# Kernel optimization log

Hardware: AMD Instinct MI355X
Metric: run time of the kernel (lower is better)

The kernel has to match this reference:

```python
import jax, jax.numpy as jnp
import numpy as np

N_NEURONS = 1024
TABLE_SIZE = 65536  # array_size (2048 quotients) * 2**remainder_size (32)
BATCH = 8192


def setup_inputs() -> dict:
    key = jax.random.key(0)
    k1, k2 = jax.random.split(key)
    # Input tuples: one fingerprint per neuron per sample, value = (quotient << rs) | remainder
    data = jax.random.randint(k1, (BATCH, N_NEURONS), 0, TABLE_SIZE, dtype=jnp.int32)
    # Dense membership/counter table equivalent to the fitted quotient filter state
    # (quotient filter with full remainders stored is an exact fingerprint set).
    table = jax.random.uniform(k2, (N_NEURONS, TABLE_SIZE), dtype=jnp.float32)
    return {"data": data, "table": table}


def reference(data, table):
    # check_member(neuron=j, quotient=data[i,j]>>rs, remainder=data[i,j]&mask)
    # == table[j, data[i,j]]; multi_rank sums memberships over neurons.
    neuron_idx = jnp.arange(table.shape[0])[None, :]          # [1, N]
    gathered = table[neuron_idx, data]                        # [B, N] gather
    response = jnp.sum(gathered, axis=1)                      # [B]
    return response
```

## Files before the change

kernel.cpp:

```cpp
#include <hip/hip_runtime.h>

#define N_NEURONS 1024
#define TABLE_SIZE 65536
#define BATCH 8192
#define NGROUPS 8
#define NPG 128
#define SPB 128
#define NCHUNK 8

__global__ __launch_bounds__(256) void qw_partial_kernel(
    const int* __restrict__ data,
    const float* __restrict__ table,
    float* __restrict__ part)
{
    const int b      = blockIdx.x;
    const int g      = b & (NGROUPS - 1);
    const int sub    = b >> 3;
    const int t      = threadIdx.x;
    const int h      = t & 1;
    const int sid    = t >> 1;
    const int sample = sub * SPB + sid;

    const int* __restrict__ dptr =
        data + (size_t)sample * N_NEURONS + g * NPG + h * 8;

    const float* __restrict__ tb =
        table + (size_t)(g * NPG + h * 8) * TABLE_SIZE;

    int4 i0 = *reinterpret_cast<const int4*>(dptr);
    int4 i1 = *reinterpret_cast<const int4*>(dptr + 4);

    float acc = 0.0f;
#pragma unroll
    for (int c = 0; c < NCHUNK; ++c) {
        const int4 c0 = i0;
        const int4 c1 = i1;
        if (c + 1 < NCHUNK) {
            const int* __restrict__ p = dptr + (c + 1) * 16;
            i0 = *reinterpret_cast<const int4*>(p);
            i1 = *reinterpret_cast<const int4*>(p + 4);
        }
        const float* __restrict__ tc = tb + (size_t)(c * 16) * TABLE_SIZE;
        const float v0 = tc[(size_t)0 * TABLE_SIZE + (size_t)c0.x];
        const float v1 = tc[(size_t)1 * TABLE_SIZE + (size_t)c0.y];
        const float v2 = tc[(size_t)2 * TABLE_SIZE + (size_t)c0.z];
        const float v3 = tc[(size_t)3 * TABLE_SIZE + (size_t)c0.w];
        const float v4 = tc[(size_t)4 * TABLE_SIZE + (size_t)c1.x];
        const float v5 = tc[(size_t)5 * TABLE_SIZE + (size_t)c1.y];
        const float v6 = tc[(size_t)6 * TABLE_SIZE + (size_t)c1.z];
        const float v7 = tc[(size_t)7 * TABLE_SIZE + (size_t)c1.w];
        acc += ((v0 + v1) + (v2 + v3)) + ((v4 + v5) + (v6 + v7));
        __syncthreads();
    }

    acc += __shfl_xor(acc, 1, 64);
    if (h == 0) {
        part[(size_t)g * BATCH + sample] = acc;
    }
}

__global__ __launch_bounds__(256) void qw_reduce_kernel(
    const float* __restrict__ part,
    float* __restrict__ out)
{
    const int i = blockIdx.x * 256 + threadIdx.x;
    float s = 0.0f;
#pragma unroll
    for (int g = 0; g < NGROUPS; ++g) {
        s += part[(size_t)g * BATCH + i];
    }
    out[i] = s;
}

__global__ __launch_bounds__(256) void qw_gather_kernel(
    const int* __restrict__ data,
    const float* __restrict__ table,
    float* __restrict__ out)
{
    const int gtid   = blockIdx.x * blockDim.x + threadIdx.x;
    const int sample = gtid >> 6;
    const int lane   = threadIdx.x & 63;
    if (sample >= BATCH) return;
    const int* __restrict__ row = data + (size_t)sample * N_NEURONS;
    float acc = 0.0f;
#pragma unroll
    for (int k = 0; k < 4; ++k) {
        const int jb = 256 * k + 4 * lane;
        const int4 idx4 = *reinterpret_cast<const int4*>(row + jb);
        acc += table[(size_t)(jb + 0) * TABLE_SIZE + idx4.x];
        acc += table[(size_t)(jb + 1) * TABLE_SIZE + idx4.y];
        acc += table[(size_t)(jb + 2) * TABLE_SIZE + idx4.z];
        acc += table[(size_t)(jb + 3) * TABLE_SIZE + idx4.w];
    }
#pragma unroll
    for (int off = 32; off >= 1; off >>= 1) acc += __shfl_xor(acc, off, 64);
    if (lane == 0) out[sample] = acc;
}

extern "C" void kernel_launch(void* const* d_in, const int* in_sizes, int n_in,
                              void* d_out, int out_size, void* d_ws, size_t ws_size,
                              hipStream_t stream)
{
    const int*   data  = (const int*)d_in[0];
    const float* table = (const float*)d_in[1];
    float*       out   = (float*)d_out;

    const size_t need = (size_t)NGROUPS * BATCH * sizeof(float);
    if (ws_size >= need) {
        float* part = (float*)d_ws;
        const int blocks = (BATCH / SPB) * NGROUPS;
        qw_partial_kernel<<<blocks, 256, 0, stream>>>(data, table, part);
        qw_reduce_kernel<<<BATCH / 256, 256, 0, stream>>>(part, out);
    } else {
        qw_gather_kernel<<<BATCH / 4, 256, 0, stream>>>(data, table, out);
    }
}
```

Measured before the change: 85.75 us.

## Double-buffer table gathers across chunks and replace syncthreads with raw barrier

```diff
diff --git a/kernel.cpp b/kernel.cpp
--- a/kernel.cpp
+++ b/kernel.cpp
@@ -7,6 +7,7 @@
 #define NPG 128
 #define SPB 128
 #define NCHUNK 8
+#define TS ((size_t)TABLE_SIZE)
 
 __global__ __launch_bounds__(256) void qw_partial_kernel(
     const int* __restrict__ data,
@@ -23,35 +24,74 @@
 
     const int* __restrict__ dptr =
         data + (size_t)sample * N_NEURONS + g * NPG + h * 8;
-
     const float* __restrict__ tb =
         table + (size_t)(g * NPG + h * 8) * TABLE_SIZE;
 
-    int4 i0 = *reinterpret_cast<const int4*>(dptr);
-    int4 i1 = *reinterpret_cast<const int4*>(dptr + 4);
+#define IDX(c)  (*reinterpret_cast<const int4*>(dptr + (c) * 16))
+#define IDX2(c) (*reinterpret_cast<const int4*>(dptr + (c) * 16 + 4))
 
+#define GATHER(d0,d1,d2,d3,d4,d5,d6,d7, c, I0, I1)                    \
+    d0 = tb[((size_t)(c) * 16 + 0) * TS + (size_t)(I0).x];            \
+    d1 = tb[((size_t)(c) * 16 + 1) * TS + (size_t)(I0).y];            \
+    d2 = tb[((size_t)(c) * 16 + 2) * TS + (size_t)(I0).z];            \
+    d3 = tb[((size_t)(c) * 16 + 3) * TS + (size_t)(I0).w];            \
+    d4 = tb[((size_t)(c) * 16 + 4) * TS + (size_t)(I1).x];            \
+    d5 = tb[((size_t)(c) * 16 + 5) * TS + (size_t)(I1).y];            \
+    d6 = tb[((size_t)(c) * 16 + 6) * TS + (size_t)(I1).z];            \
+    d7 = tb[((size_t)(c) * 16 + 7) * TS + (size_t)(I1).w];
+
+#define SUM8(d0,d1,d2,d3,d4,d5,d6,d7) \
+    (((d0 + d1) + (d2 + d3)) + ((d4 + d5) + (d6 + d7)))
+
+    int4 p0 = IDX(0), p1 = IDX2(0);
+    int4 q0 = IDX(1), q1 = IDX2(1);
+
+    float A0,A1,A2,A3,A4,A5,A6,A7;
+    float B0,B1,B2,B3,B4,B5,B6,B7;
     float acc = 0.0f;
-#pragma unroll
-    for (int c = 0; c < NCHUNK; ++c) {
-        const int4 c0 = i0;
-        const int4 c1 = i1;
-        if (c + 1 < NCHUNK) {
-            const int* __restrict__ p = dptr + (c + 1) * 16;
-            i0 = *reinterpret_cast<const int4*>(p);
-            i1 = *reinterpret_cast<const int4*>(p + 4);
-        }
-        const float* __restrict__ tc = tb + (size_t)(c * 16) * TABLE_SIZE;
-        const float v0 = tc[(size_t)0 * TABLE_SIZE + (size_t)c0.x];
-        const float v1 = tc[(size_t)1 * TABLE_SIZE + (size_t)c0.y];
-        const float v2 = tc[(size_t)2 * TABLE_SIZE + (size_t)c0.z];
-        const float v3 = tc[(size_t)3 * TABLE_SIZE + (size_t)c0.w];
-        const float v4 = tc[(size_t)4 * TABLE_SIZE + (size_t)c1.x];
-        const float v5 = tc[(size_t)5 * TABLE_SIZE + (size_t)c1.y];
-        const float v6 = tc[(size_t)6 * TABLE_SIZE + (size_t)c1.z];
-        const float v7 = tc[(size_t)7 * TABLE_SIZE + (size_t)c1.w];
-        acc += ((v0 + v1) + (v2 + v3)) + ((v4 + v5) + (v6 + v7));
-        __syncthreads();
-    }
+
+    GATHER(A0,A1,A2,A3,A4,A5,A6,A7, 0, p0, p1);
+
+    GATHER(B0,B1,B2,B3,B4,B5,B6,B7, 1, q0, q1);
+    p0 = IDX(2); p1 = IDX2(2);
+    __builtin_amdgcn_s_barrier();
+    acc += SUM8(A0,A1,A2,A3,A4,A5,A6,A7);
+
+    GATHER(A0,A1,A2,A3,A4,A5,A6,A7, 2, p0, p1);
+    q0 = IDX(3); q1 = IDX2(3);
+    __builtin_amdgcn_s_barrier();
+    acc += SUM8(B0,B1,B2,B3,B4,B5,B6,B7);
+
+    GATHER(B0,B1,B2,B3,B4,B5,B6,B7, 3, q0, q1);
+    p0 = IDX(4); p1 = IDX2(4);
+    __builtin_amdgcn_s_barrier();
+    acc += SUM8(A0,A1,A2,A3,A4,A5,A6,A7);
+
+    GATHER(A0,A1,A2,A3,A4,A5,A6,A7, 4, p0, p1);
+    q0 = IDX(5); q1 = IDX2(5);
+    __builtin_amdgcn_s_barrier();
+    acc += SUM8(B0,B1,B2,B3,B4,B5,B6,B7);
+
+    GATHER(B0,B1,B2,B3,B4,B5,B6,B7, 5, q0, q1);
+    p0 = IDX(6); p1 = IDX2(6);
+    __builtin_amdgcn_s_barrier();
+    acc += SUM8(A0,A1,A2,A3,A4,A5,A6,A7);
+
+    GATHER(A0,A1,A2,A3,A4,A5,A6,A7, 6, p0, p1);
+    q0 = IDX(7); q1 = IDX2(7);
+    __builtin_amdgcn_s_barrier();
+    acc += SUM8(B0,B1,B2,B3,B4,B5,B6,B7);
+
+    GATHER(B0,B1,B2,B3,B4,B5,B6,B7, 7, q0, q1);
+    __builtin_amdgcn_s_barrier();
+    acc += SUM8(A0,A1,A2,A3,A4,A5,A6,A7);
+
+    acc += SUM8(B0,B1,B2,B3,B4,B5,B6,B7);
+
+#undef GATHER
+#undef SUM8
+#undef IDX
+#undef IDX2
 
     acc += __shfl_xor(acc, 1, 64);
     if (h == 0) {
```

Measured after the change: 84.17 us. Within noise of the previous version (-1.8%).

## Add grid-wide per-group barriers to keep blocks in lockstep over table chunks

Applied to the files above, without the earlier changes.

```diff
diff --git a/kernel.cpp b/kernel.cpp
--- a/kernel.cpp
+++ b/kernel.cpp
@@ -5,13 +5,22 @@
 #define BATCH 8192
 #define NGROUPS 8
 #define NPG 128
-#define SPB 128
+#define SPB 256
+#define TPB 512
 #define NCHUNK 8
+#define NBLK ((BATCH / SPB) * NGROUPS)
+#define BPG (NBLK / NGROUPS)
+#define TS ((size_t)TABLE_SIZE)
 
-__global__ __launch_bounds__(256) void qw_partial_kernel(
+__global__ void qw_init_kernel(unsigned* __restrict__ bar) {
+    bar[threadIdx.x] = 0u;
+}
+
+__global__ __launch_bounds__(TPB) void qw_partial_kernel(
     const int* __restrict__ data,
     const float* __restrict__ table,
-    float* __restrict__ part)
+    float* __restrict__ part,
+    unsigned* __restrict__ bar)
 {
     const int b      = blockIdx.x;
     const int g      = b & (NGROUPS - 1);
@@ -23,35 +32,52 @@
 
     const int* __restrict__ dptr =
         data + (size_t)sample * N_NEURONS + g * NPG + h * 8;
-
     const float* __restrict__ tb =
         table + (size_t)(g * NPG + h * 8) * TABLE_SIZE;
+    unsigned* __restrict__ gbar = bar + g * 32;
 
-    int4 i0 = *reinterpret_cast<const int4*>(dptr);
-    int4 i1 = *reinterpret_cast<const int4*>(dptr + 4);
+#define IDX(c)  (*reinterpret_cast<const int4*>(dptr + (c) * 16))
+#define IDX2(c) (*reinterpret_cast<const int4*>(dptr + (c) * 16 + 4))
 
+    int4 i0 = IDX(0), i1 = IDX2(0);
     float acc = 0.0f;
+
 #pragma unroll
     for (int c = 0; c < NCHUNK; ++c) {
         const int4 c0 = i0;
         const int4 c1 = i1;
         if (c + 1 < NCHUNK) {
-            const int* __restrict__ p = dptr + (c + 1) * 16;
-            i0 = *reinterpret_cast<const int4*>(p);
-            i1 = *reinterpret_cast<const int4*>(p + 4);
+            i0 = IDX(c + 1);
+            i1 = IDX2(c + 1);
         }
         const float* __restrict__ tc = tb + (size_t)(c * 16) * TABLE_SIZE;
-        const float v0 = tc[(size_t)0 * TABLE_SIZE + (size_t)c0.x];
-        const float v1 = tc[(size_t)1 * TABLE_SIZE + (size_t)c0.y];
-        const float v2 = tc[(size_t)2 * TABLE_SIZE + (size_t)c0.z];
-        const float v3 = tc[(size_t)3 * TABLE_SIZE + (size_t)c0.w];
-        const float v4 = tc[(size_t)4 * TABLE_SIZE + (size_t)c1.x];
-        const float v5 = tc[(size_t)5 * TABLE_SIZE + (size_t)c1.y];
-        const float v6 = tc[(size_t)6 * TABLE_SIZE + (size_t)c1.z];
-        const float v7 = tc[(size_t)7 * TABLE_SIZE + (size_t)c1.w];
+        const float v0 = tc[(size_t)0 * TS + (size_t)c0.x];
+        const float v1 = tc[(size_t)1 * TS + (size_t)c0.y];
+        const float v2 = tc[(size_t)2 * TS + (size_t)c0.z];
+        const float v3 = tc[(size_t)3 * TS + (size_t)c0.w];
+        const float v4 = tc[(size_t)4 * TS + (size_t)c1.x];
+        const float v5 = tc[(size_t)5 * TS + (size_t)c1.y];
+        const float v6 = tc[(size_t)6 * TS + (size_t)c1.z];
+        const float v7 = tc[(size_t)7 * TS + (size_t)c1.w];
         acc += ((v0 + v1) + (v2 + v3)) + ((v4 + v5) + (v6 + v7));
-        __syncthreads();
+
+        if (c + 1 < NCHUNK) {
+            __syncthreads();
+            if (t == 0) {
+                __hip_atomic_fetch_add(&gbar[c], 1u, __ATOMIC_ACQ_REL,
+                                       __HIP_MEMORY_SCOPE_AGENT);
+                int budget = 20000;
+                while (__hip_atomic_load(&gbar[c], __ATOMIC_ACQUIRE,
+                                         __HIP_MEMORY_SCOPE_AGENT) < (unsigned)BPG
+                       && --budget) {
+                    __builtin_amdgcn_s_sleep(2);
+                }
+            }
+            __syncthreads();
+        }
     }
+#undef IDX
+#undef IDX2
 
     acc += __shfl_xor(acc, 1, 64);
     if (h == 0) {
@@ -87,10 +113,10 @@
     for (int k = 0; k < 4; ++k) {
         const int jb = 256 * k + 4 * lane;
         const int4 idx4 = *reinterpret_cast<const int4*>(row + jb);
-        acc += table[(size_t)(jb + 0) * TABLE_SIZE + idx4.x];
-        acc += table[(size_t)(jb + 1) * TABLE_SIZE + idx4.y];
-        acc += table[(size_t)(jb + 2) * TABLE_SIZE + idx4.z];
-        acc += table[(size_t)(jb + 3) * TABLE_SIZE + idx4.w];
+        acc += table[(size_t)(jb + 0) * TS + idx4.x];
+        acc += table[(size_t)(jb + 1) * TS + idx4.y];
+        acc += table[(size_t)(jb + 2) * TS + idx4.z];
+        acc += table[(size_t)(jb + 3) * TS + idx4.w];
     }
 #pragma unroll
     for (int off = 32; off >= 1; off >>= 1) acc += __shfl_xor(acc, off, 64);
@@ -105,11 +131,13 @@
     const float* table = (const float*)d_in[1];
     float*       out   = (float*)d_out;
 
-    const size_t need = (size_t)NGROUPS * BATCH * sizeof(float);
-    if (ws_size >= need) {
-        float* part = (float*)d_ws;
-        const int blocks = (BATCH / SPB) * NGROUPS;
-        qw_partial_kernel<<<blocks, 256, 0, stream>>>(data, table, part);
+    const size_t part_bytes = (size_t)NGROUPS * BATCH * sizeof(float);
+    const size_t bar_bytes  = (size_t)NGROUPS * 32 * sizeof(unsigned);
+    if (ws_size >= part_bytes + bar_bytes) {
+        float*    part = (float*)d_ws;
+        unsigned* bar  = (unsigned*)((char*)d_ws + part_bytes);
+        qw_init_kernel<<<1, NGROUPS * 32, 0, stream>>>(bar);
+        qw_partial_kernel<<<NBLK, TPB, 0, stream>>>(data, table, part, bar);
         qw_reduce_kernel<<<BATCH / 256, 256, 0, stream>>>(part, out);
     } else {
         qw_gather_kernel<<<BATCH / 4, 256, 0, stream>>>(data, table, out);
```

Measured after the change: 180.3 us. 110% more time.

## Split partial gather into eight phase launches to confine table working set

Applied to the files above, without the earlier changes.

```diff
diff --git a/kernel.cpp b/kernel.cpp
--- a/kernel.cpp
+++ b/kernel.cpp
@@ -6,12 +6,16 @@
 #define NGROUPS 8
 #define NPG 128
 #define SPB 128
-#define NCHUNK 8
+#define TPB 256
+#define NPHASE 8
+#define NBLK ((BATCH / SPB) * NGROUPS)
+#define TS ((size_t)TABLE_SIZE)
 
-__global__ __launch_bounds__(256) void qw_partial_kernel(
+__global__ __launch_bounds__(TPB) void qw_phase_kernel(
     const int* __restrict__ data,
     const float* __restrict__ table,
-    float* __restrict__ part)
+    float* __restrict__ part,
+    int phase)
 {
     const int b      = blockIdx.x;
     const int g      = b & (NGROUPS - 1);
@@ -21,41 +25,33 @@
     const int sid    = t >> 1;
     const int sample = sub * SPB + sid;
 
-    const int* __restrict__ dptr =
-        data + (size_t)sample * N_NEURONS + g * NPG + h * 8;
+    const int jbase  = g * NPG + phase * 16 + h * 8;
 
-    const float* __restrict__ tb =
-        table + (size_t)(g * NPG + h * 8) * TABLE_SIZE;
+    const int* __restrict__ dptr = data + (size_t)sample * N_NEURONS + jbase;
+    const int4 i0 = *reinterpret_cast<const int4*>(dptr);
+    const int4 i1 = *reinterpret_cast<const int4*>(dptr + 4);
 
-    int4 i0 = *reinterpret_cast<const int4*>(dptr);
-    int4 i1 = *reinterpret_cast<const int4*>(dptr + 4);
+    const float* __restrict__ tb = table + (size_t)jbase * TABLE_SIZE;
 
-    float acc = 0.0f;
-#pragma unroll
-    for (int c = 0; c < NCHUNK; ++c) {
-        const int4 c0 = i0;
-        const int4 c1 = i1;
-        if (c + 1 < NCHUNK) {
-            const int* __restrict__ p = dptr + (c + 1) * 16;
-            i0 = *reinterpret_cast<const int4*>(p);
-            i1 = *reinterpret_cast<const int4*>(p + 4);
-        }
-        const float* __restrict__ tc = tb + (size_t)(c * 16) * TABLE_SIZE;
-        const float v0 = tc[(size_t)0 * TABLE_SIZE + (size_t)c0.x];
-        const float v1 = tc[(size_t)1 * TABLE_SIZE + (size_t)c0.y];
-        const float v2 = tc[(size_t)2 * TABLE_SIZE + (size_t)c0.z];
-        const float v3 = tc[(size_t)3 * TABLE_SIZE + (size_t)c0.w];
-        const float v4 = tc[(size_t)4 * TABLE_SIZE + (size_t)c1.x];
-        const float v5 = tc[(size_t)5 * TABLE_SIZE + (size_t)c1.y];
-        const float v6 = tc[(size_t)6 * TABLE_SIZE + (size_t)c1.z];
-        const float v7 = tc[(size_t)7 * TABLE_SIZE + (size_t)c1.w];
-        acc += ((v0 + v1) + (v2 + v3)) + ((v4 + v5) + (v6 + v7));
-        __syncthreads();
-    }
+    const float v0 = tb[(size_t)0 * TS + (size_t)i0.x];
+    const float v1 = tb[(size_t)1 * TS + (size_t)i0.y];
+    const float v2 = tb[(size_t)2 * TS + (size_t)i0.z];
+    const float v3 = tb[(size_t)3 * TS + (size_t)i0.w];
+    const float v4 = tb[(size_t)4 * TS + (size_t)i1.x];
+    const float v5 = tb[(size_t)5 * TS + (size_t)i1.y];
+    const float v6 = tb[(size_t)6 * TS + (size_t)i1.z];
+    const float v7 = tb[(size_t)7 * TS + (size_t)i1.w];
+    float acc = ((v0 + v1) + (v2 + v3)) + ((v4 + v5) + (v6 + v7));
 
     acc += __shfl_xor(acc, 1, 64);
+
     if (h == 0) {
-        part[(size_t)g * BATCH + sample] = acc;
+        float* dst = part + (size_t)g * BATCH + sample;
+        if (phase == 0) {
+            *dst = acc;
+        } else {
+            *dst += acc;
+        }
     }
 }
 
@@ -87,10 +83,10 @@
     for (int k = 0; k < 4; ++k) {
         const int jb = 256 * k + 4 * lane;
         const int4 idx4 = *reinterpret_cast<const int4*>(row + jb);
-        acc += table[(size_t)(jb + 0) * TABLE_SIZE + idx4.x];
-        acc += table[(size_t)(jb + 1) * TABLE_SIZE + idx4.y];
-        acc += table[(size_t)(jb + 2) * TABLE_SIZE + idx4.z];
-        acc += table[(size_t)(jb + 3) * TABLE_SIZE + idx4.w];
+        acc += table[(size_t)(jb + 0) * TS + idx4.x];
+        acc += table[(size_t)(jb + 1) * TS + idx4.y];
+        acc += table[(size_t)(jb + 2) * TS + idx4.z];
+        acc += table[(size_t)(jb + 3) * TS + idx4.w];
     }
 #pragma unroll
     for (int off = 32; off >= 1; off >>= 1) acc += __shfl_xor(acc, off, 64);
@@ -105,11 +101,12 @@
     const float* table = (const float*)d_in[1];
     float*       out   = (float*)d_out;
 
-    const size_t need = (size_t)NGROUPS * BATCH * sizeof(float);
-    if (ws_size >= need) {
+    const size_t part_bytes = (size_t)NGROUPS * BATCH * sizeof(float);
+    if (ws_size >= part_bytes) {
         float* part = (float*)d_ws;
-        const int blocks = (BATCH / SPB) * NGROUPS;
-        qw_partial_kernel<<<blocks, 256, 0, stream>>>(data, table, part);
+        for (int p = 0; p < NPHASE; ++p) {
+            qw_phase_kernel<<<NBLK, TPB, 0, stream>>>(data, table, part, p);
+        }
         qw_reduce_kernel<<<BATCH / 256, 256, 0, stream>>>(part, out);
     } else {
         qw_gather_kernel<<<BATCH / 4, 256, 0, stream>>>(data, table, out);
```

New measurement: 101.6 us. +18.5%, slower.
